# Optimization experiments

Measured on AMD Instinct MI355X. Metric: run time of the kernel, lower is better.

## Reference

```python
import jax, jax.numpy as jnp
import numpy as np

C_DIM = 640
CTX_DIM = 768
N_HEADS = 8

def setup_inputs() -> dict:
    key = jax.random.key(0)
    ks = jax.random.split(key, 12)
    B, C, H, W = 16, C_DIM, 64, 64
    T = 77
    s_c = 1.0 / np.sqrt(C)
    s_ctx = 1.0 / np.sqrt(CTX_DIM)
    return {
        "x": jax.random.normal(ks[0], (B, C, H, W), jnp.float32),
        "context": jax.random.normal(ks[1], (B, T, CTX_DIM), jnp.float32),
        "Wq": jax.random.normal(ks[2], (C, C), jnp.float32) * s_c,
        "bq": jnp.zeros((C,), jnp.float32),
        "Wk": jax.random.normal(ks[3], (CTX_DIM, C), jnp.float32) * s_ctx,
        "bk": jnp.zeros((C,), jnp.float32),
        "Wv": jax.random.normal(ks[4], (CTX_DIM, C), jnp.float32) * s_ctx,
        "bv": jnp.zeros((C,), jnp.float32),
        "Wo": jax.random.normal(ks[5], (C, C), jnp.float32) * s_c,
        "bo": jnp.zeros((C,), jnp.float32),
    }

def reference(x, context, Wq, bq, Wk, bk, Wv, bv, Wo, bo):
    B, C, H, W = x.shape
    h = N_HEADS
    d = C // h
    scale = d ** (-0.5)
    # (B,C,H,W) -> (B, HW, C)
    xs = x.reshape(B, C, H * W).transpose(0, 2, 1)
    q = xs @ Wq + bq                      # (B, HW, C)
    k = context @ Wk + bk                 # (B, T, C)
    v = context @ Wv + bv                 # (B, T, C)
    q = q.reshape(B, H * W, h, d).transpose(0, 2, 1, 3)  # (B,h,HW,d)
    k = k.reshape(B, -1, h, d).transpose(0, 2, 1, 3)      # (B,h,T,d)
    v = v.reshape(B, -1, h, d).transpose(0, 2, 1, 3)      # (B,h,T,d)
    scores = jnp.einsum('bhnd,bhtd->bhnt', q, k) * scale  # (B,h,HW,T)
    attn = jax.nn.softmax(scores, axis=-1)
    out = jnp.einsum('bhnt,bhtd->bhnd', attn, v)           # (B,h,HW,d)
    out = out.transpose(0, 2, 1, 3).reshape(B, H * W, C)
    out = out @ Wo + bo                                    # (B, HW, C)
    return out.transpose(0, 2, 1).reshape(B, C, H, W)
```

## Files before the change

kernel.cpp:

```cpp
#include <hip/hip_runtime.h>
#include <hip/hip_fp16.h>

typedef _Float16 half_t;
typedef _Float16 f16x8 __attribute__((ext_vector_type(8)));
typedef _Float16 f16x4 __attribute__((ext_vector_type(4)));
typedef float f32x4 __attribute__((ext_vector_type(4)));

#define NB   16
#define CD   640
#define HWD  4096
#define TT   77
#define CTXD 768
#define NH   8
#define DH   80
#define DP   96

#define GLOAD16(gp, lp)                                                        \
  __builtin_amdgcn_global_load_lds(                                            \
      (const __attribute__((address_space(1))) void*)(gp),                     \
      (__attribute__((address_space(3))) void*)(lp), 16, 0, 0)

__device__ inline void xcd_panel_map(int j, int& panel, int& nblk) {
  const int xcd = j & 7, slot = j >> 3;
  panel = (slot / 5) * 8 + xcd;
  nblk = slot % 5;
}

__global__ __launch_bounds__(256) void xpose_kernel(
    const float* __restrict__ x, half_t* __restrict__ xt) {
  __shared__ half_t tile[64][72];
  const float* s = x + (long)blockIdx.z * CD * HWD;
  half_t* d = xt + (long)blockIdx.z * HWD * CD;
  const int r0 = blockIdx.y * 64;
  const int c0 = blockIdx.x * 64;
  const int t = threadIdx.x;
  const int rr = t >> 4, cc = (t & 15) * 4;
#pragma unroll
  for (int j = 0; j < 4; ++j) {
    const int r = rr + j * 16;
    float4 v = *reinterpret_cast<const float4*>(&s[(long)(r0 + r) * HWD + c0 + cc]);
    tile[cc + 0][r] = (half_t)v.x;
    tile[cc + 1][r] = (half_t)v.y;
    tile[cc + 2][r] = (half_t)v.z;
    tile[cc + 3][r] = (half_t)v.w;
  }
  __syncthreads();
  const int cr = t >> 2, rc = (t & 3) * 16;
  half_t* dp = &d[(long)(c0 + cr) * CD + r0 + rc];
  *reinterpret_cast<int4*>(dp)     = *reinterpret_cast<const int4*>(&tile[cr][rc]);
  *reinterpret_cast<int4*>(dp + 8) = *reinterpret_cast<const int4*>(&tile[cr][rc + 8]);
}

__global__ __launch_bounds__(256) void wtrans_kernel(
    const float* __restrict__ Wq, const float* __restrict__ Wk,
    const float* __restrict__ Wv, const float* __restrict__ Wo,
    half_t* __restrict__ WqT, half_t* __restrict__ WkT,
    half_t* __restrict__ WvT, half_t* __restrict__ WoT) {
  __shared__ half_t tile[64][72];
  const int z = blockIdx.z;
  const float* src = (z == 0) ? Wq : (z == 1) ? Wk : (z == 2) ? Wv : Wo;
  half_t* dst      = (z == 0) ? WqT : (z == 1) ? WkT : (z == 2) ? WvT : WoT;
  const int R = (z == 1 || z == 2) ? CTXD : CD;
  const int r0 = blockIdx.y * 64, c0 = blockIdx.x * 64;
  if (r0 >= R) return;
  const int t = threadIdx.x;
  const int rr = t >> 4, cc = (t & 15) * 4;
#pragma unroll
  for (int j = 0; j < 4; ++j) {
    const int r = rr + j * 16;
    float4 v = *reinterpret_cast<const float4*>(&src[(long)(r0 + r) * CD + c0 + cc]);
    tile[cc + 0][r] = (half_t)v.x;
    tile[cc + 1][r] = (half_t)v.y;
    tile[cc + 2][r] = (half_t)v.z;
    tile[cc + 3][r] = (half_t)v.w;
  }
  __syncthreads();
  const int cr = t >> 2, rc = (t & 3) * 16;
  half_t* dp = &dst[(long)(c0 + cr) * R + r0 + rc];
  *reinterpret_cast<int4*>(dp)     = *reinterpret_cast<const int4*>(&tile[cr][rc]);
  *reinterpret_cast<int4*>(dp + 8) = *reinterpret_cast<const int4*>(&tile[cr][rc + 8]);
}

__global__ __launch_bounds__(256) void kv_kernel(
    const float* __restrict__ ctx,
    const half_t* __restrict__ WkT, const half_t* __restrict__ WvT,
    const float* __restrict__ bk, const float* __restrict__ bv,
    half_t* __restrict__ k_ws, half_t* __restrict__ vT_ws) {
  __shared__ half_t C_sm[80][32];
  const int n0 = blockIdx.x * 64;
  const int b  = blockIdx.y;
  const int kv = blockIdx.z;
  const half_t* WT  = kv ? WvT : WkT;
  const float* bias = kv ? bv : bk;
  const int tid = threadIdx.x;
  const int wave = tid >> 6, lane = tid & 63, g = lane >> 4, ln = lane & 15;

  f32x4 acc[5];
#pragma unroll
  for (int i = 0; i < 5; ++i) acc[i] = (f32x4){0.f, 0.f, 0.f, 0.f};

  for (int k0 = 0; k0 < CTXD; k0 += 32) {
    if (k0) __syncthreads();
    for (int i = tid; i < 320; i += 256) {
      const int r = i >> 2, c8 = (i & 3) * 8;
      f16x8 hv = {0, 0, 0, 0, 0, 0, 0, 0};
      if (r < TT) {
        const float* cp = ctx + ((long)b * TT + r) * CTXD + k0 + c8;
        float4 c0v = *reinterpret_cast<const float4*>(cp);
        float4 c1v = *reinterpret_cast<const float4*>(cp + 4);
        hv[0] = (half_t)c0v.x; hv[1] = (half_t)c0v.y;
        hv[2] = (half_t)c0v.z; hv[3] = (half_t)c0v.w;
        hv[4] = (half_t)c1v.x; hv[5] = (half_t)c1v.y;
        hv[6] = (half_t)c1v.z; hv[7] = (half_t)c1v.w;
      }
      *reinterpret_cast<f16x8*>(&C_sm[r][c8]) = hv;
    }
    __syncthreads();
    f16x8 bfr = *reinterpret_cast<const f16x8*>(
        &WT[(long)(n0 + wave * 16 + ln) * CTXD + k0 + g * 8]);
#pragma unroll
    for (int mt = 0; mt < 5; ++mt) {
      f16x8 afr = *reinterpret_cast<const f16x8*>(&C_sm[mt * 16 + ln][g * 8]);
      acc[mt] = __builtin_amdgcn_mfma_f32_16x16x32_f16(afr, bfr, acc[mt], 0, 0, 0);
    }
  }

  const int n = n0 + wave * 16 + ln;
  const float bsv = bias[n];
  const int h = n / DH, dd = n % DH;
  if (kv == 0) {
#pragma unroll
    for (int mt = 0; mt < 5; ++mt)
#pragma unroll
      for (int r = 0; r < 4; ++r) {
        const int t = mt * 16 + g * 4 + r;
        k_ws[(((long)b * NH + h) * 80 + t) * DP + dd] = (half_t)(acc[mt][r] + bsv);
      }
  } else {
#pragma unroll
    for (int mt = 0; mt < 5; ++mt) {
      const int t0 = mt * 16 + g * 4;
      f16x4 v4;
#pragma unroll
      for (int r = 0; r < 4; ++r) v4[r] = (half_t)(acc[mt][r] + bsv);
      *reinterpret_cast<f16x4*>(&vT_ws[(((long)b * NH + h) * 80 + dd) * DP + t0]) = v4;
    }
  }
}

template <int EPI>
__global__ __launch_bounds__(256, 3) void pgemm_kernel(
    const half_t* __restrict__ A, const half_t* __restrict__ BT,
    const float* __restrict__ bias, void* __restrict__ outp) {
  __shared__ __align__(16) half_t A_sm[3][128 * 32];
  __shared__ __align__(16) half_t B_sm[3][128 * 32];
  const int tid = threadIdx.x;
  const int lane = tid & 63, wave = tid >> 6;
  const int g = lane >> 4, ln = lane & 15;
  const int wm = wave >> 1, wn = wave & 1;

  int panel, nblk;
  xcd_panel_map(blockIdx.x, panel, nblk);
  const long m0 = (long)panel * 128;
  const int n0 = nblk * 128;

  const int srow = tid >> 2;
  const int sk8 = ((tid & 3) ^ ((tid >> 3) & 3)) * 8;
  const half_t* ag0 = A + (m0 + srow) * CD + sk8;
  const half_t* ag1 = ag0 + 64 * CD;
  const half_t* bg0 = BT + (long)(n0 + srow) * CD + sk8;
  const half_t* bg1 = bg0 + 64 * CD;

  const int rs8 = (g ^ ((ln >> 1) & 3)) * 8;

  f32x4 acc[4][4];
#pragma unroll
  for (int i = 0; i < 4; ++i)
#pragma unroll
    for (int j = 0; j < 4; ++j) acc[i][j] = (f32x4){0.f, 0.f, 0.f, 0.f};

#define STAGE_AB(buf, kt)                                              \
  do {                                                                 \
    GLOAD16(ag0 + (long)(kt) * 32, &A_sm[buf][wave * 512]);            \
    GLOAD16(ag1 + (long)(kt) * 32, &A_sm[buf][2048 + wave * 512]);     \
    GLOAD16(bg0 + (long)(kt) * 32, &B_sm[buf][wave * 512]);            \
    GLOAD16(bg1 + (long)(kt) * 32, &B_sm[buf][2048 + wave * 512]);     \
  } while (0)

  STAGE_AB(0, 0);
  STAGE_AB(1, 1);

  const int nk = CD / 32;
  for (int kt = 0; kt < nk; ++kt) {
    const int cur = kt % 3;
    if (kt + 2 < nk) {
      STAGE_AB((kt + 2) % 3, kt + 2);
      asm volatile("s_waitcnt vmcnt(8)" ::: "memory");
    } else if (kt + 1 < nk) {
      asm volatile("s_waitcnt vmcnt(4)" ::: "memory");
    } else {
      asm volatile("s_waitcnt vmcnt(0)" ::: "memory");
    }
    __builtin_amdgcn_s_barrier();
    __builtin_amdgcn_sched_barrier(0);
    f16x8 af[4], bf[4];
#pragma unroll
    for (int mi = 0; mi < 4; ++mi)
      af[mi] = *reinterpret_cast<const f16x8*>(
          &A_sm[cur][(wm * 64 + mi * 16 + ln) * 32 + rs8]);
#pragma unroll
    for (int ni = 0; ni < 4; ++ni)
      bf[ni] = *reinterpret_cast<const f16x8*>(
          &B_sm[cur][(wn * 64 + ni * 16 + ln) * 32 + rs8]);
    __builtin_amdgcn_s_setprio(1);
#pragma unroll
    for (int mi = 0; mi < 4; ++mi)
#pragma unroll
      for (int ni = 0; ni < 4; ++ni)
        acc[mi][ni] = __builtin_amdgcn_mfma_f32_16x16x32_f16(af[mi], bf[ni], acc[mi][ni], 0, 0, 0);
    __builtin_amdgcn_s_setprio(0);
    __builtin_amdgcn_s_barrier();
  }

  if (EPI == 0) {
    half_t* O = (half_t*)outp;
#pragma unroll
    for (int ni = 0; ni < 4; ++ni) {
      const int n = n0 + wn * 64 + ni * 16 + ln;
      const float bvv = bias[n];
#pragma unroll
      for (int mi = 0; mi < 4; ++mi) {
        const long m = m0 + wm * 64 + mi * 16 + g * 4;
        f32x4 v = acc[mi][ni];
#pragma unroll
        for (int r = 0; r < 4; ++r)
          O[(m + r) * CD + n] = (half_t)(v[r] + bvv);
      }
    }
  } else {
    float* O = (float*)outp;
#pragma unroll
    for (int mi = 0; mi < 4; ++mi) {
      const long m = m0 + wm * 64 + mi * 16 + g * 4;
      const long bb = m >> 12;
      const int p = (int)(m & 4095);
#pragma unroll
      for (int ni = 0; ni < 4; ++ni) {
        const int n = n0 + wn * 64 + ni * 16 + ln;
        const float bvv = bias[n];
        f32x4 v = acc[mi][ni];
        float4 o4 = make_float4(v[0] + bvv, v[1] + bvv, v[2] + bvv, v[3] + bvv);
        *reinterpret_cast<float4*>(&O[((bb * CD + n) << 12) + p]) = o4;
      }
    }
  }
#undef STAGE_AB
}

__global__ __launch_bounds__(512) void attn_kernel(
    const half_t* __restrict__ q_ws, const half_t* __restrict__ k_ws,
    const half_t* __restrict__ vT_ws, half_t* __restrict__ attn_ws) {
  __shared__ half_t K_sm[80][DP];
  __shared__ half_t V_sm[80][DP];
  __shared__ half_t Q_sm[128][DP];
  const int p0 = blockIdx.x * 128;
  const int h  = blockIdx.y;
  const int b  = blockIdx.z;
  const int tid = threadIdx.x, wave = tid >> 6, lane = tid & 63;
  const int g = lane >> 4, ln = lane & 15;

  const half_t* kp = k_ws  + ((long)b * NH + h) * 80 * DP;
  const half_t* vp = vT_ws + ((long)b * NH + h) * 80 * DP;
  for (int i = tid; i < 960; i += 512) {
    reinterpret_cast<int4*>(K_sm)[i] = reinterpret_cast<const int4*>(kp)[i];
    reinterpret_cast<int4*>(V_sm)[i] = reinterpret_cast<const int4*>(vp)[i];
  }
  for (int i = tid; i < 1536; i += 512) {
    const int r = i / 12, c8 = i % 12;
    int4 v = make_int4(0, 0, 0, 0);
    if (c8 < 10)
      v = *reinterpret_cast<const int4*>(
          q_ws + ((long)(b * HWD + p0 + r)) * CD + h * DH + c8 * 8);
    *reinterpret_cast<int4*>(&Q_sm[r][c8 * 8]) = v;
  }
  __syncthreads();

  f32x4 s[5];
#pragma unroll
  for (int i = 0; i < 5; ++i) s[i] = (f32x4){0.f, 0.f, 0.f, 0.f};
#pragma unroll
  for (int ks = 0; ks < 3; ++ks) {
    f16x8 bq = *reinterpret_cast<const f16x8*>(&Q_sm[wave * 16 + ln][ks * 32 + g * 8]);
#pragma unroll
    for (int mt = 0; mt < 5; ++mt) {
      f16x8 ak = *reinterpret_cast<const f16x8*>(&K_sm[mt * 16 + ln][ks * 32 + g * 8]);
      s[mt] = __builtin_amdgcn_mfma_f32_16x16x32_f16(ak, bq, s[mt], 0, 0, 0);
    }
  }

  const float sc = 0.11180339887498949f;
  float mx = -1e30f;
#pragma unroll
  for (int mt = 0; mt < 5; ++mt)
#pragma unroll
    for (int r = 0; r < 4; ++r) {
      const int t = mt * 16 + g * 4 + r;
      const float v = s[mt][r] * sc;
      s[mt][r] = v;
      if (t < TT) mx = fmaxf(mx, v);
    }
  mx = fmaxf(mx, __shfl_xor(mx, 16));
  mx = fmaxf(mx, __shfl_xor(mx, 32));
  float e[5][4];
  float sum = 0.f;
#pragma unroll
  for (int mt = 0; mt < 5; ++mt)
#pragma unroll
    for (int r = 0; r < 4; ++r) {
      const int t = mt * 16 + g * 4 + r;
      float ev = 0.f;
      if (t < TT) { ev = __expf(s[mt][r] - mx); sum += ev; }
      e[mt][r] = ev;
    }
  sum += __shfl_xor(sum, 16);
  sum += __shfl_xor(sum, 32);
  const float inv = 1.f / sum;
#pragma unroll
  for (int mt = 0; mt < 5; ++mt) {
    f16x4 pv;
#pragma unroll
    for (int r = 0; r < 4; ++r) pv[r] = (half_t)(e[mt][r] * inv);
    *reinterpret_cast<f16x4*>(&Q_sm[wave * 16 + ln][mt * 16 + g * 4]) = pv;
  }

  f32x4 o[5];
#pragma unroll
  for (int i = 0; i < 5; ++i) o[i] = (f32x4){0.f, 0.f, 0.f, 0.f};
#pragma unroll
  for (int ks = 0; ks < 3; ++ks) {
    f16x8 bp = *reinterpret_cast<const f16x8*>(&Q_sm[wave * 16 + ln][ks * 32 + g * 8]);
#pragma unroll
    for (int mt = 0; mt < 5; ++mt) {
      f16x8 av = *reinterpret_cast<const f16x8*>(&V_sm[mt * 16 + ln][ks * 32 + g * 8]);
      o[mt] = __builtin_amdgcn_mfma_f32_16x16x32_f16(av, bp, o[mt], 0, 0, 0);
    }
  }

  half_t* op = attn_ws + ((long)(b * HWD + p0 + wave * 16 + ln)) * CD + h * DH;
#pragma unroll
  for (int mt = 0; mt < 5; ++mt) {
    f16x4 v4;
#pragma unroll
    for (int r = 0; r < 4; ++r) v4[r] = (half_t)o[mt][r];
    *reinterpret_cast<f16x4*>(&op[mt * 16 + g * 4]) = v4;
  }
}

extern "C" void kernel_launch(void* const* d_in, const int* in_sizes, int n_in,
                              void* d_out, int out_size, void* d_ws, size_t ws_size,
                              hipStream_t stream) {
  const float* x   = (const float*)d_in[0];
  const float* ctx = (const float*)d_in[1];
  const float* Wq  = (const float*)d_in[2];
  const float* bq  = (const float*)d_in[3];
  const float* Wk  = (const float*)d_in[4];
  const float* bk  = (const float*)d_in[5];
  const float* Wv  = (const float*)d_in[6];
  const float* bv  = (const float*)d_in[7];
  const float* Wo  = (const float*)d_in[8];
  const float* bo  = (const float*)d_in[9];
  float* out = (float*)d_out;

  char* ws = (char*)d_ws;
  size_t off = 0;
  auto alloc = [&](size_t bytes) {
    void* p = ws + off;
    off += (bytes + 255) & ~(size_t)255;
    return p;
  };
  half_t* WqT  = (half_t*)alloc((size_t)CD * CD * 2);
  half_t* WkT  = (half_t*)alloc((size_t)CD * CTXD * 2);
  half_t* WvT  = (half_t*)alloc((size_t)CD * CTXD * 2);
  half_t* WoT  = (half_t*)alloc((size_t)CD * CD * 2);
  half_t* kws  = (half_t*)alloc((size_t)NB * NH * 80 * DP * 2);
  half_t* vTws = (half_t*)alloc((size_t)NB * NH * 80 * DP * 2);
  half_t* xt   = (half_t*)alloc((size_t)NB * HWD * CD * 2);
  half_t* q    = (half_t*)alloc((size_t)NB * HWD * CD * 2);
  half_t* attn = xt;

  hipMemsetAsync(kws, 0, (size_t)2 * NB * NH * 80 * DP * 2, stream);

  wtrans_kernel<<<dim3(CD / 64, CTXD / 64, 4), 256, 0, stream>>>(
      Wq, Wk, Wv, Wo, WqT, WkT, WvT, WoT);

  kv_kernel<<<dim3(CD / 64, NB, 2), 256, 0, stream>>>(ctx, WkT, WvT, bk, bv, kws, vTws);

  xpose_kernel<<<dim3(HWD / 64, CD / 64, NB), 256, 0, stream>>>(x, xt);

  pgemm_kernel<0><<<(CD / 128) * ((NB * HWD) / 128), 256, 0, stream>>>(
      xt, WqT, bq, q);

  attn_kernel<<<dim3(HWD / 128, NH, NB), 512, 0, stream>>>(q, kws, vTws, attn);

  pgemm_kernel<1><<<(CD / 128) * ((NB * HWD) / 128), 256, 0, stream>>>(
      attn, WoT, bo, out);
}
```

Baseline: 317.3 us.

## Fuse input transpose and fp16 conversion into the Q projection GEMM

Removes the separate transpose kernel that wrote a half-precision transposed copy of x. The Q GEMM now reads fp32 x directly in its channel-major layout, converts it to fp16 in registers, and writes it transposed into swizzled shared memory, with a register-staged, software-pipelined prologue and main loop. This saves a full write and re-read of a 16x4096x640 fp16 intermediate. In exchange the GEMM's A loads are wider fp32 loads, it does more register pressure and conversion work, and it relies on hand-tuned waitcnt ordering. The attention output buffer now gets its own allocation.

New measurement: 315.3 us. About the same (-0.6%).

```diff
diff --git a/kernel.cpp b/kernel.cpp
--- a/kernel.cpp
+++ b/kernel.cpp
@@ -24,31 +24,6 @@
   const int xcd = j & 7, slot = j >> 3;
   panel = (slot / 5) * 8 + xcd;
   nblk = slot % 5;
-}
-
-__global__ __launch_bounds__(256) void xpose_kernel(
-    const float* __restrict__ x, half_t* __restrict__ xt) {
-  __shared__ half_t tile[64][72];
-  const float* s = x + (long)blockIdx.z * CD * HWD;
-  half_t* d = xt + (long)blockIdx.z * HWD * CD;
-  const int r0 = blockIdx.y * 64;
-  const int c0 = blockIdx.x * 64;
-  const int t = threadIdx.x;
-  const int rr = t >> 4, cc = (t & 15) * 4;
-#pragma unroll
-  for (int j = 0; j < 4; ++j) {
-    const int r = rr + j * 16;
-    float4 v = *reinterpret_cast<const float4*>(&s[(long)(r0 + r) * HWD + c0 + cc]);
-    tile[cc + 0][r] = (half_t)v.x;
-    tile[cc + 1][r] = (half_t)v.y;
-    tile[cc + 2][r] = (half_t)v.z;
-    tile[cc + 3][r] = (half_t)v.w;
-  }
-  __syncthreads();
-  const int cr = t >> 2, rc = (t & 3) * 16;
-  half_t* dp = &d[(long)(c0 + cr) * CD + r0 + rc];
-  *reinterpret_cast<int4*>(dp)     = *reinterpret_cast<const int4*>(&tile[cr][rc]);
-  *reinterpret_cast<int4*>(dp + 8) = *reinterpret_cast<const int4*>(&tile[cr][rc + 8]);
 }
 
 __global__ __launch_bounds__(256) void wtrans_kernel(
@@ -148,10 +123,155 @@
   }
 }
 
-template <int EPI>
-__global__ __launch_bounds__(256, 3) void pgemm_kernel(
+__global__ __launch_bounds__(256, 3) void qgemm_kernel(
+    const float* __restrict__ x, const half_t* __restrict__ BT,
+    const float* __restrict__ bias, half_t* __restrict__ outp) {
+  __shared__ __align__(16) half_t A_sm[3][128 * 32];
+  __shared__ __align__(16) half_t B_sm[3][128 * 32];
+  const int tid = threadIdx.x;
+  const int lane = tid & 63, wave = tid >> 6;
+  const int g = lane >> 4, ln = lane & 15;
+  const int wm = wave >> 1, wn = wave & 1;
+
+  int panel, nblk;
+  xcd_panel_map(blockIdx.x, panel, nblk);
+  const long m0 = (long)panel * 128;
+  const int n0 = nblk * 128;
+  const int b  = (int)(m0 >> 12);
+  const int p0 = (int)(m0 & 4095);
+
+  const int pg = tid & 31;
+  const int cg = tid >> 5;
+  const float* xg = x + ((long)b * CD + cg * 4) * HWD + p0 + pg * 4;
+  const int cgh = cg >> 1, cgs = (cg & 1) * 4;
+  const int wb01 = (pg * 4) * 32     + (cgh ^ ((2 * pg) & 3)) * 8     + cgs;
+  const int wb23 = (pg * 4 + 2) * 32 + (cgh ^ ((2 * pg + 1) & 3)) * 8 + cgs;
+
+  const int srow = tid >> 2;
+  const int sk8 = ((tid & 3) ^ ((tid >> 3) & 3)) * 8;
+  const half_t* bg0 = BT + (long)(n0 + srow) * CD + sk8;
+  const half_t* bg1 = bg0 + 64 * CD;
+
+  const int rs8 = (g ^ ((ln >> 1) & 3)) * 8;
+
+  f32x4 acc[4][4];
+#pragma unroll
+  for (int i = 0; i < 4; ++i)
+#pragma unroll
+    for (int j = 0; j < 4; ++j) acc[i][j] = (f32x4){0.f, 0.f, 0.f, 0.f};
+
+  float4 ra0, ra1, ra2, ra3;
+  float4 rb0, rb1, rb2, rb3;
+
+#define LOADA(R0, R1, R2, R3, xp)                                     \
+  do {                                                                \
+    R0 = *reinterpret_cast<const float4*>(xp);                        \
+    R1 = *reinterpret_cast<const float4*>((xp) + HWD);                \
+    R2 = *reinterpret_cast<const float4*>((xp) + 2 * HWD);            \
+    R3 = *reinterpret_cast<const float4*>((xp) + 3 * HWD);            \
+  } while (0)
+
+#define LOADB(kt, buf)                                                \
+  do {                                                                \
+    GLOAD16(bg0 + (long)(kt) * 32, &B_sm[buf][wave * 512]);           \
+    GLOAD16(bg1 + (long)(kt) * 32, &B_sm[buf][2048 + wave * 512]);    \
+  } while (0)
+
+#define CVTW(R0, R1, R2, R3, buf)                                     \
+  do {                                                                \
+    half_t* as_ = &A_sm[buf][0];                                      \
+    f16x4 w_;                                                         \
+    w_[0] = (half_t)R0.x; w_[1] = (half_t)R1.x;                       \
+    w_[2] = (half_t)R2.x; w_[3] = (half_t)R3.x;                       \
+    *reinterpret_cast<f16x4*>(as_ + wb01) = w_;                       \
+    w_[0] = (half_t)R0.y; w_[1] = (half_t)R1.y;                       \
+    w_[2] = (half_t)R2.y; w_[3] = (half_t)R3.y;                       \
+    *reinterpret_cast<f16x4*>(as_ + wb01 + 32) = w_;                  \
+    w_[0] = (half_t)R0.z; w_[1] = (half_t)R1.z;                       \
+    w_[2] = (half_t)R2.z; w_[3] = (half_t)R3.z;                       \
+    *reinterpret_cast<f16x4*>(as_ + wb23) = w_;                       \
+    w_[0] = (half_t)R0.w; w_[1] = (half_t)R1.w;                       \
+    w_[2] = (half_t)R2.w; w_[3] = (half_t)R3.w;                       \
+    *reinterpret_cast<f16x4*>(as_ + wb23 + 32) = w_;                  \
+  } while (0)
+
+#define COMPUTE(buf)                                                  \
+  do {                                                                \
+    __builtin_amdgcn_s_barrier();                                     \
+    __builtin_amdgcn_sched_barrier(0);                                \
+    f16x8 af[4], bf[4];                                               \
+    _Pragma("unroll")                                                 \
+    for (int mi = 0; mi < 4; ++mi)                                    \
+      af[mi] = *reinterpret_cast<const f16x8*>(                       \
+          &A_sm[buf][(wm * 64 + mi * 16 + ln) * 32 + rs8]);           \
+    _Pragma("unroll")                                                 \
+    for (int ni = 0; ni < 4; ++ni)                                    \
+      bf[ni] = *reinterpret_cast<const f16x8*>(                       \
+          &B_sm[buf][(wn * 64 + ni * 16 + ln) * 32 + rs8]);           \
+    __builtin_amdgcn_s_setprio(1);                                    \
+    _Pragma("unroll")                                                 \
+    for (int mi = 0; mi < 4; ++mi)                                    \
+      _Pragma("unroll")                                               \
+      for (int ni = 0; ni < 4; ++ni)                                  \
+        acc[mi][ni] = __builtin_amdgcn_mfma_f32_16x16x32_f16(         \
+            af[mi], bf[ni], acc[mi][ni], 0, 0, 0);                    \
+    __builtin_amdgcn_s_setprio(0);                                    \
+    __builtin_amdgcn_s_barrier();                                     \
+  } while (0)
+
+  LOADA(ra0, ra1, ra2, ra3, xg);
+  LOADB(0, 0);
+  LOADA(rb0, rb1, rb2, rb3, xg + 32 * HWD);
+  LOADB(1, 1);
+  asm volatile("s_waitcnt vmcnt(8)" ::: "memory");
+  CVTW(ra0, ra1, ra2, ra3, 0);
+
+  const float* xk = xg + 64 * HWD;
+  for (int k2 = 0; k2 < 18; k2 += 2) {
+    const int c0 = k2 % 3, c1 = (k2 + 1) % 3, c2 = (k2 + 2) % 3;
+    LOADA(ra0, ra1, ra2, ra3, xk);
+    LOADB(k2 + 2, c2);
+    asm volatile("s_waitcnt vmcnt(8)" ::: "memory");
+    CVTW(rb0, rb1, rb2, rb3, c1);
+    asm volatile("s_waitcnt vmcnt(6) lgkmcnt(0)" ::: "memory");
+    COMPUTE(c0);
+    LOADA(rb0, rb1, rb2, rb3, xk + 32 * HWD);
+    LOADB(k2 + 3, c0);
+    asm volatile("s_waitcnt vmcnt(8)" ::: "memory");
+    CVTW(ra0, ra1, ra2, ra3, c2);
+    asm volatile("s_waitcnt vmcnt(6) lgkmcnt(0)" ::: "memory");
+    COMPUTE(c1);
+    xk += 64 * HWD;
+  }
+  asm volatile("s_waitcnt vmcnt(2)" ::: "memory");
+  CVTW(rb0, rb1, rb2, rb3, 1);
+  asm volatile("s_waitcnt vmcnt(0) lgkmcnt(0)" ::: "memory");
+  COMPUTE(0);
+  COMPUTE(1);
+
+  half_t* O = outp;
+#pragma unroll
+  for (int ni = 0; ni < 4; ++ni) {
+    const int n = n0 + wn * 64 + ni * 16 + ln;
+    const float bvv = bias[n];
+#pragma unroll
+    for (int mi = 0; mi < 4; ++mi) {
+      const long m = m0 + wm * 64 + mi * 16 + g * 4;
+      f32x4 v = acc[mi][ni];
+#pragma unroll
+      for (int r = 0; r < 4; ++r)
+        O[(m + r) * CD + n] = (half_t)(v[r] + bvv);
+    }
+  }
+#undef LOADA
+#undef LOADB
+#undef CVTW
+#undef COMPUTE
+}
+
+__global__ __launch_bounds__(256, 3) void ogemm_kernel(
     const half_t* __restrict__ A, const half_t* __restrict__ BT,
-    const float* __restrict__ bias, void* __restrict__ outp) {
+    const float* __restrict__ bias, float* __restrict__ outp) {
   __shared__ __align__(16) half_t A_sm[3][128 * 32];
   __shared__ __align__(16) half_t B_sm[3][128 * 32];
   const int tid = threadIdx.x;
@@ -222,36 +342,19 @@
     __builtin_amdgcn_s_barrier();
   }
 
-  if (EPI == 0) {
-    half_t* O = (half_t*)outp;
+  float* O = outp;
+#pragma unroll
+  for (int mi = 0; mi < 4; ++mi) {
+    const long m = m0 + wm * 64 + mi * 16 + g * 4;
+    const long bb = m >> 12;
+    const int p = (int)(m & 4095);
 #pragma unroll
     for (int ni = 0; ni < 4; ++ni) {
       const int n = n0 + wn * 64 + ni * 16 + ln;
       const float bvv = bias[n];
-#pragma unroll
-      for (int mi = 0; mi < 4; ++mi) {
-        const long m = m0 + wm * 64 + mi * 16 + g * 4;
-        f32x4 v = acc[mi][ni];
-#pragma unroll
-        for (int r = 0; r < 4; ++r)
-          O[(m + r) * CD + n] = (half_t)(v[r] + bvv);
-      }
-    }
-  } else {
-    float* O = (float*)outp;
-#pragma unroll
-    for (int mi = 0; mi < 4; ++mi) {
-      const long m = m0 + wm * 64 + mi * 16 + g * 4;
-      const long bb = m >> 12;
-      const int p = (int)(m & 4095);
-#pragma unroll
-      for (int ni = 0; ni < 4; ++ni) {
-        const int n = n0 + wn * 64 + ni * 16 + ln;
-        const float bvv = bias[n];
-        f32x4 v = acc[mi][ni];
-        float4 o4 = make_float4(v[0] + bvv, v[1] + bvv, v[2] + bvv, v[3] + bvv);
-        *reinterpret_cast<float4*>(&O[((bb * CD + n) << 12) + p]) = o4;
-      }
+      f32x4 v = acc[mi][ni];
+      float4 o4 = make_float4(v[0] + bvv, v[1] + bvv, v[2] + bvv, v[3] + bvv);
+      *reinterpret_cast<float4*>(&O[((bb * CD + n) << 12) + p]) = o4;
     }
   }
 #undef STAGE_AB
@@ -384,9 +487,8 @@
   half_t* WoT  = (half_t*)alloc((size_t)CD * CD * 2);
   half_t* kws  = (half_t*)alloc((size_t)NB * NH * 80 * DP * 2);
   half_t* vTws = (half_t*)alloc((size_t)NB * NH * 80 * DP * 2);
-  half_t* xt   = (half_t*)alloc((size_t)NB * HWD * CD * 2);
   half_t* q    = (half_t*)alloc((size_t)NB * HWD * CD * 2);
-  half_t* attn = xt;
+  half_t* attn = (half_t*)alloc((size_t)NB * HWD * CD * 2);
 
   hipMemsetAsync(kws, 0, (size_t)2 * NB * NH * 80 * DP * 2, stream);
 
@@ -395,13 +497,11 @@
 
   kv_kernel<<<dim3(CD / 64, NB, 2), 256, 0, stream>>>(ctx, WkT, WvT, bk, bv, kws, vTws);
 
-  xpose_kernel<<<dim3(HWD / 64, CD / 64, NB), 256, 0, stream>>>(x, xt);
-
-  pgemm_kernel<0><<<(CD / 128) * ((NB * HWD) / 128), 256, 0, stream>>>(
-      xt, WqT, bq, q);
+  qgemm_kernel<<<(CD / 128) * ((NB * HWD) / 128), 256, 0, stream>>>(
+      x, WqT, bq, q);
 
   attn_kernel<<<dim3(HWD / 128, NH, NB), 512, 0, stream>>>(q, kws, vTws, attn);
 
-  pgemm_kernel<1><<<(CD / 128) * ((NB * HWD) / 128), 256, 0, stream>>>(
+  ogemm_kernel<<<(CD / 128) * ((NB * HWD) / 128), 256, 0, stream>>>(
       attn, WoT, bo, out);
 }
```
